# Kernel optimization log

Measured on AMD Instinct MI355X. Metric: run time of the kernel, lower is better.

The kernel has to match this reference:

```python
import jax, jax.numpy as jnp
import numpy as np

N_NODES = 100000
N_EDGES = 1600000
IN_F = 64
HID = 64
OUT_F = 64


def _param(key, shape, fan_in):
    return jax.random.normal(key, shape, dtype=jnp.float32) * (1.0 / np.sqrt(fan_in))


def setup_inputs() -> dict:
    key = jax.random.key(0)
    ks = jax.random.split(key, 12)
    features = jax.random.normal(ks[0], (N_NODES, IN_F), dtype=jnp.float32)
    src = jax.random.randint(ks[1], (N_EDGES,), 0, N_NODES, dtype=jnp.int32)
    dst = jax.random.randint(ks[2], (N_EDGES,), 0, N_NODES, dtype=jnp.int32)
    dims = [(IN_F, HID), (HID, HID), (HID, OUT_F)]
    inp = {"features": features, "src": src, "dst": dst}
    for i, (din, dout) in enumerate(dims):
        inp[f"W_self{i}"] = _param(ks[3 + 3 * i], (din, dout), din)
        inp[f"W_neigh{i}"] = _param(ks[4 + 3 * i], (din, dout), din)
        inp[f"b{i}"] = jnp.zeros((dout,), dtype=jnp.float32)
    return inp


def _sage_layer(h, src, dst, W_self, W_neigh, b, deg_inv, n_nodes, act):
    # mean aggregation over in-neighbors: gather src feats, segment-sum into dst
    msum = jax.ops.segment_sum(h[src], dst, num_segments=n_nodes)  # [N, d]
    h_neigh = msum * deg_inv  # mean (zero-degree nodes -> 0, matching DGL)
    out = h @ W_self + h_neigh @ W_neigh + b
    return jax.nn.relu(out) if act else out


def reference(features, src, dst, W_self0, W_neigh0, b0, W_self1, W_neigh1, b1, W_self2, W_neigh2, b2):
    n = features.shape[0]
    deg = jax.ops.segment_sum(jnp.ones((src.shape[0],), jnp.float32), dst, num_segments=n)
    deg_inv = (1.0 / jnp.maximum(deg, 1.0))[:, None]  # [N, 1]
    h = _sage_layer(features, src, dst, W_self0, W_neigh0, b0, deg_inv, n, act=True)
    h = _sage_layer(h, src, dst, W_self1, W_neigh1, b1, deg_inv, n, act=True)
    h = _sage_layer(h, src, dst, W_self2, W_neigh2, b2, deg_inv, n, act=False)
    return h
```

## Files before the change

### kernel.cpp

```cpp
#include <hip/hip_runtime.h>

#define NF 64
#define BUCKET 128
#define MAXB 8192
#define EPB 4096

typedef __attribute__((ext_vector_type(8))) short bf16x8;
typedef __attribute__((ext_vector_type(4))) float f32x4;

__device__ __forceinline__ float bf2f(unsigned short x) {
    union { unsigned int u; float f; } v; v.u = ((unsigned int)x) << 16; return v.f;
}
__device__ __forceinline__ unsigned short f2bf(float x) {
    union { float f; unsigned int u; } v; v.f = x;
    unsigned int r = (v.u + 0x7FFFu + ((v.u >> 16) & 1u)) >> 16;
    return (unsigned short)r;
}


__global__ __launch_bounds__(256) void bhist_kernel(const int* __restrict__ dst,
                                                    int* __restrict__ bins,
                                                    int n_edges, int nb) {
    __shared__ int h[MAXB];
    for (int i = threadIdx.x; i < nb; i += 256) h[i] = 0;
    __syncthreads();
    int base = blockIdx.x * EPB;
    int lim = min(base + EPB, n_edges);
    for (int i = base + threadIdx.x; i < lim; i += 256)
        atomicAdd(&h[dst[i] >> 7], 1);
    __syncthreads();
    for (int i = threadIdx.x; i < nb; i += 256) {
        int v = h[i];
        if (v) atomicAdd(&bins[i], v);
    }
}

__global__ __launch_bounds__(1024) void bscan_kernel(const int* __restrict__ bins,
                                                     int* __restrict__ bptr,
                                                     int* __restrict__ gcur, int nb) {
    __shared__ int sd[1024];
    int carry = 0;
    if (threadIdx.x == 0) bptr[0] = 0;
    for (int base = 0; base < nb; base += 1024) {
        int i = base + threadIdx.x;
        int v = (i < nb) ? bins[i] : 0;
        sd[threadIdx.x] = v;
        __syncthreads();
        for (int off = 1; off < 1024; off <<= 1) {
            int t = (threadIdx.x >= off) ? sd[threadIdx.x - off] : 0;
            __syncthreads();
            sd[threadIdx.x] += t;
            __syncthreads();
        }
        if (i < nb) {
            int ex = carry + sd[threadIdx.x] - v;
            bptr[i + 1] = carry + sd[threadIdx.x];
            gcur[i] = ex;
        }
        int last = sd[1023];
        __syncthreads();
        carry += last;
    }
}

__global__ __launch_bounds__(256) void bscatter_kernel(const int* __restrict__ src,
                                                       const int* __restrict__ dst,
                                                       int* __restrict__ gcur,
                                                       unsigned* __restrict__ bedges,
                                                       int n_edges, int nb) {
    __shared__ int h[MAXB];
    for (int i = threadIdx.x; i < nb; i += 256) h[i] = 0;
    __syncthreads();
    int base = blockIdx.x * EPB;
    int myDst[16], mySrc[16];
#pragma unroll
    for (int k = 0; k < 16; ++k) {
        int i = base + k * 256 + threadIdx.x;
        if (i < n_edges) {
            myDst[k] = dst[i];
            mySrc[k] = src[i];
            atomicAdd(&h[myDst[k] >> 7], 1);
        } else {
            myDst[k] = -1;
        }
    }
    __syncthreads();
    for (int i = threadIdx.x; i < nb; i += 256) {
        int v = h[i];
        h[i] = v ? atomicAdd(&gcur[i], v) : 0;
    }
    __syncthreads();
#pragma unroll
    for (int k = 0; k < 16; ++k) {
        if (myDst[k] >= 0) {
            int bin = myDst[k] >> 7;
            int pos = atomicAdd(&h[bin], 1);
            bedges[pos] = ((unsigned)mySrc[k] << 7) | (unsigned)(myDst[k] & 127);
        }
    }
}

__global__ __launch_bounds__(256) void bfinal_kernel(
    const unsigned* __restrict__ bedges, const int* __restrict__ bptr,
    int* __restrict__ row_ptr, float* __restrict__ deginv,
    int* __restrict__ col, int n_nodes, int n_edges, int nb) {
    __shared__ int cnt[BUCKET];
    __shared__ int sa[BUCKET], sb2[BUCKET];
    int tid = threadIdx.x;
    int b = blockIdx.x;
    int beg = bptr[b], end = bptr[b + 1];
    if (tid < BUCKET) cnt[tid] = 0;
    __syncthreads();
    for (int i = beg + tid; i < end; i += 256)
        atomicAdd(&cnt[bedges[i] & (BUCKET - 1)], 1);
    __syncthreads();
    if (tid < BUCKET) sa[tid] = cnt[tid];
    __syncthreads();
    int* pin = sa; int* pout = sb2;
    for (int off = 1; off < BUCKET; off <<= 1) {
        if (tid < BUCKET) pout[tid] = pin[tid] + ((tid >= off) ? pin[tid - off] : 0);
        __syncthreads();
        int* t = pin; pin = pout; pout = t;
    }
    int nodeBase = b * BUCKET;
    if (tid < BUCKET && nodeBase + tid < n_nodes) {
        row_ptr[nodeBase + tid] = beg + (tid ? pin[tid - 1] : 0);
        deginv[nodeBase + tid] = 1.0f / fmaxf((float)cnt[tid], 1.0f);
    }
    if (b == nb - 1 && tid == 0) row_ptr[n_nodes] = n_edges;
    __syncthreads();
    if (tid < BUCKET) cnt[tid] = 0;
    __syncthreads();
    for (int i = beg + tid; i < end; i += 256) {
        unsigned e = bedges[i];
        int d = e & (BUCKET - 1);
        int pos = beg + (d ? pin[d - 1] : 0) + atomicAdd(&cnt[d], 1);
        col[pos] = (int)(e >> 7);
    }
}


__global__ void convert_kernel(const float* __restrict__ in, unsigned short* __restrict__ X, int n_nodes) {
    int t = blockIdx.x * blockDim.x + threadIdx.x;
    int total = n_nodes * 16;
    if (t >= total) return;
    int n = t >> 4, g = t & 15;
    float4 v = *reinterpret_cast<const float4*>(in + (size_t)n * 64 + g * 4);
    ushort4 o;
    o.x = f2bf(v.x); o.y = f2bf(v.y); o.z = f2bf(v.z); o.w = f2bf(v.w);
    *reinterpret_cast<ushort4*>(X + (size_t)n * 128 + g * 4) = o;
}

__global__ void wtrans_kernel(const float* __restrict__ Ws, const float* __restrict__ Wn,
                              unsigned short* __restrict__ WT) {
    int t = blockIdx.x * blockDim.x + threadIdx.x;
    if (t >= 64 * 128) return;
    int j = t >> 7, k = t & 127;
    float v = (k < 64) ? Ws[k * 64 + j] : Wn[(k - 64) * 64 + j];
    WT[(size_t)j * 128 + k] = f2bf(v);
}

__global__ __launch_bounds__(256) void aggregate_bf16_kernel(
    unsigned short* __restrict__ X, const int* __restrict__ row_ptr, const int* __restrict__ col,
    const float* __restrict__ deginv, int n_nodes) {
    int lane = threadIdx.x & 63;
    int wid = threadIdx.x >> 6;
    int n = blockIdx.x * 4 + wid;
    if (n >= n_nodes) return;
    int beg = row_ptr[n], end = row_ptr[n + 1];
    float acc = 0.f;
    int i = beg;
    for (; i + 3 < end; i += 4) {
        int s0 = col[i], s1 = col[i + 1], s2 = col[i + 2], s3 = col[i + 3];
        float v0 = bf2f(X[(size_t)s0 * 128 + lane]);
        float v1 = bf2f(X[(size_t)s1 * 128 + lane]);
        float v2 = bf2f(X[(size_t)s2 * 128 + lane]);
        float v3 = bf2f(X[(size_t)s3 * 128 + lane]);
        acc += (v0 + v1) + (v2 + v3);
    }
    for (; i < end; ++i) acc += bf2f(X[(size_t)col[i] * 128 + lane]);
    X[(size_t)n * 128 + 64 + lane] = f2bf(acc * deginv[n]);
}

__global__ __launch_bounds__(256) void linear_mfma_kernel(
    const unsigned short* __restrict__ X, const unsigned short* __restrict__ WT,
    const float* __restrict__ bias, unsigned short* __restrict__ outBf,
    float* __restrict__ outF32, int n_nodes, int do_relu) {
    int lane = threadIdx.x & 63;
    int wid = threadIdx.x >> 6;
    int l15 = lane & 15;
    int lg = lane >> 4;

    bf16x8 wf[4][4];
#pragma unroll
    for (int ft = 0; ft < 4; ++ft)
#pragma unroll
        for (int ks = 0; ks < 4; ++ks)
            wf[ft][ks] = *reinterpret_cast<const bf16x8*>(
                WT + (size_t)(ft * 16 + l15) * 128 + ks * 32 + lg * 8);

    float4 bv[4];
#pragma unroll
    for (int ft = 0; ft < 4; ++ft)
        bv[ft] = *reinterpret_cast<const float4*>(bias + ft * 16 + lg * 4);

    int tiles = (n_nodes + 15) >> 4;
    for (int tile = blockIdx.x * 4 + wid; tile < tiles; tile += gridDim.x * 4) {
        int nodeBase = tile * 16;
        int nrow = nodeBase + l15;
        int rrow = nrow < n_nodes ? nrow : n_nodes - 1;

        bf16x8 xf[4];
#pragma unroll
        for (int ks = 0; ks < 4; ++ks)
            xf[ks] = *reinterpret_cast<const bf16x8*>(X + (size_t)rrow * 128 + ks * 32 + lg * 8);

        f32x4 acc[4];
#pragma unroll
        for (int ft = 0; ft < 4; ++ft) acc[ft] = (f32x4){0.f, 0.f, 0.f, 0.f};
#pragma unroll
        for (int ks = 0; ks < 4; ++ks) {
#pragma unroll
            for (int ft = 0; ft < 4; ++ft)
                acc[ft] = __builtin_amdgcn_mfma_f32_16x16x32_bf16(wf[ft][ks], xf[ks], acc[ft], 0, 0, 0);
        }

        if (nrow < n_nodes) {
#pragma unroll
            for (int ft = 0; ft < 4; ++ft) {
                float4 v;
                v.x = acc[ft][0] + bv[ft].x;
                v.y = acc[ft][1] + bv[ft].y;
                v.z = acc[ft][2] + bv[ft].z;
                v.w = acc[ft][3] + bv[ft].w;
                if (do_relu) {
                    v.x = fmaxf(v.x, 0.f); v.y = fmaxf(v.y, 0.f);
                    v.z = fmaxf(v.z, 0.f); v.w = fmaxf(v.w, 0.f);
                }
                int fbase = ft * 16 + lg * 4;
                if (outF32) {
                    *reinterpret_cast<float4*>(outF32 + (size_t)nrow * 64 + fbase) = v;
                } else {
                    ushort4 o;
                    o.x = f2bf(v.x); o.y = f2bf(v.y); o.z = f2bf(v.z); o.w = f2bf(v.w);
                    *reinterpret_cast<ushort4*>(outBf + (size_t)nrow * 128 + fbase) = o;
                }
            }
        }
    }
}


__global__ void deg_kernel(const int* __restrict__ dst, float* __restrict__ deg, int n_edges) {
    int e = blockIdx.x * blockDim.x + threadIdx.x;
    if (e < n_edges) unsafeAtomicAdd(&deg[dst[e]], 1.0f);
}

__global__ void inv_kernel(float* __restrict__ deg, int n) {
    int i = blockIdx.x * blockDim.x + threadIdx.x;
    if (i < n) deg[i] = 1.0f / fmaxf(deg[i], 1.0f);
}

__global__ __launch_bounds__(256) void scatter_kernel(
    const float* __restrict__ h, const int* __restrict__ src, const int* __restrict__ dst,
    float* __restrict__ agg, int n_edges) {
    int t = blockIdx.x * blockDim.x + threadIdx.x;
    int e = t >> 4;
    if (e >= n_edges) return;
    int q = (t & 15) * 4;
    int s = src[e];
    int d = dst[e];
    float4 v = *reinterpret_cast<const float4*>(h + (size_t)s * NF + q);
    float* o = agg + (size_t)d * NF + q;
    unsafeAtomicAdd(o + 0, v.x);
    unsafeAtomicAdd(o + 1, v.y);
    unsafeAtomicAdd(o + 2, v.z);
    unsafeAtomicAdd(o + 3, v.w);
}

__global__ __launch_bounds__(256) void linear_kernel(
    const float* __restrict__ h, const float* __restrict__ agg, const float* __restrict__ deginv,
    const float* __restrict__ Ws, const float* __restrict__ Wn, const float* __restrict__ bias,
    float* __restrict__ out, int n_nodes, int do_relu) {
    __shared__ float sWs[NF * NF];
    __shared__ float sWn[NF * NF];
    __shared__ float sb[NF];
    for (int i = threadIdx.x; i < NF * NF; i += 256) {
        sWs[i] = Ws[i];
        sWn[i] = Wn[i];
    }
    if (threadIdx.x < NF) sb[threadIdx.x] = bias[threadIdx.x];
    __syncthreads();
    int j = threadIdx.x & 63;
    int sub = threadIdx.x >> 6;
    for (int n = blockIdx.x * 4 + sub; n < n_nodes; n += gridDim.x * 4) {
        const float4* hr = reinterpret_cast<const float4*>(h + (size_t)n * NF);
        const float4* ar = reinterpret_cast<const float4*>(agg + (size_t)n * NF);
        float accS = 0.f, accN = 0.f;
#pragma unroll
        for (int k4 = 0; k4 < 16; ++k4) {
            float4 hv = hr[k4];
            float4 av = ar[k4];
            int kb = k4 * 4;
            accS += hv.x * sWs[(kb + 0) * NF + j];
            accN += av.x * sWn[(kb + 0) * NF + j];
            accS += hv.y * sWs[(kb + 1) * NF + j];
            accN += av.y * sWn[(kb + 1) * NF + j];
            accS += hv.z * sWs[(kb + 2) * NF + j];
            accN += av.z * sWn[(kb + 2) * NF + j];
            accS += hv.w * sWs[(kb + 3) * NF + j];
            accN += av.w * sWn[(kb + 3) * NF + j];
        }
        float val = accS + deginv[n] * accN + sb[j];
        if (do_relu) val = fmaxf(val, 0.f);
        out[(size_t)n * NF + j] = val;
    }
}


extern "C" void kernel_launch(void* const* d_in, const int* in_sizes, int n_in,
                              void* d_out, int out_size, void* d_ws, size_t ws_size,
                              hipStream_t stream) {
    const float* features = (const float*)d_in[0];
    const int* src = (const int*)d_in[1];
    const int* dst = (const int*)d_in[2];
    const float* Ws0 = (const float*)d_in[3];
    const float* Wn0 = (const float*)d_in[4];
    const float* b0  = (const float*)d_in[5];
    const float* Ws1 = (const float*)d_in[6];
    const float* Wn1 = (const float*)d_in[7];
    const float* b1  = (const float*)d_in[8];
    const float* Ws2 = (const float*)d_in[9];
    const float* Wn2 = (const float*)d_in[10];
    const float* b2  = (const float*)d_in[11];

    const int n_nodes = in_sizes[0] / NF;
    const int n_edges = in_sizes[1];
    float* out = (float*)d_out;

    const int nb = (n_nodes + BUCKET - 1) / BUCKET;
    const size_t alignNB = (((size_t)nb + 1) * 4 + 255) / 256 * 256;
    const size_t alignN = (((size_t)n_nodes + 64) * 4 + 255) / 256 * 256;
    const size_t alignE = ((size_t)n_edges * 4 + 255) / 256 * 256;
    const size_t xBytes = ((size_t)n_nodes * 128 * 2 + 255) / 256 * 256;
    const size_t wtBytes = 64 * 128 * 2;

    dim3 blk(256);
    const int nEB = (n_edges + EPB - 1) / EPB;
    const int waveBlocks = (n_nodes + 3) / 4;
    const int tiles = (n_nodes + 15) / 16;
    const int linBlocks = ((tiles + 3) / 4 < 640) ? (tiles + 3) / 4 : 640;

    const size_t need = 3 * alignNB + 2 * alignN + alignE + 2 * xBytes + 3 * wtBytes;
    const bool outFits = (size_t)out_size * sizeof(float) >= (size_t)n_edges * sizeof(unsigned);

    if (ws_size >= need && nb <= MAXB && n_nodes < (1 << 25) && outFits) {
        char* ws = (char*)d_ws;
        int* bins     = (int*)ws;
        int* bptr     = (int*)(ws + alignNB);
        int* gcur     = (int*)(ws + 2 * alignNB);
        int* row_ptr  = (int*)(ws + 3 * alignNB);
        float* deginv = (float*)(ws + 3 * alignNB + alignN);
        int* col      = (int*)(ws + 3 * alignNB + 2 * alignN);
        unsigned short* X0  = (unsigned short*)(ws + 3 * alignNB + 2 * alignN + alignE);
        unsigned short* X1  = (unsigned short*)((char*)X0 + xBytes);
        unsigned short* WT0 = (unsigned short*)((char*)X1 + xBytes);
        unsigned short* WT1 = WT0 + 64 * 128;
        unsigned short* WT2 = WT1 + 64 * 128;
        unsigned* bedges = (unsigned*)d_out;

        hipMemsetAsync(bins, 0, (size_t)nb * sizeof(int), stream);
        bhist_kernel<<<nEB, blk, 0, stream>>>(dst, bins, n_edges, nb);
        bscan_kernel<<<1, 1024, 0, stream>>>(bins, bptr, gcur, nb);
        bscatter_kernel<<<nEB, blk, 0, stream>>>(src, dst, gcur, bedges, n_edges, nb);
        bfinal_kernel<<<nb, blk, 0, stream>>>(bedges, bptr, row_ptr, deginv, col, n_nodes, n_edges, nb);

        convert_kernel<<<(n_nodes * 16 + 255) / 256, blk, 0, stream>>>(features, X0, n_nodes);
        wtrans_kernel<<<32, blk, 0, stream>>>(Ws0, Wn0, WT0);
        wtrans_kernel<<<32, blk, 0, stream>>>(Ws1, Wn1, WT1);
        wtrans_kernel<<<32, blk, 0, stream>>>(Ws2, Wn2, WT2);

        aggregate_bf16_kernel<<<waveBlocks, blk, 0, stream>>>(X0, row_ptr, col, deginv, n_nodes);
        linear_mfma_kernel<<<linBlocks, blk, 0, stream>>>(X0, WT0, b0, X1, nullptr, n_nodes, 1);
        aggregate_bf16_kernel<<<waveBlocks, blk, 0, stream>>>(X1, row_ptr, col, deginv, n_nodes);
        linear_mfma_kernel<<<linBlocks, blk, 0, stream>>>(X1, WT1, b1, X0, nullptr, n_nodes, 1);
        aggregate_bf16_kernel<<<waveBlocks, blk, 0, stream>>>(X0, row_ptr, col, deginv, n_nodes);
        linear_mfma_kernel<<<linBlocks, blk, 0, stream>>>(X0, WT2, b2, nullptr, out, n_nodes, 0);
    } else {
        char* ws = (char*)d_ws;
        size_t degBytes = (((size_t)n_nodes * 4) + 255) / 256 * 256;
        float* deg = (float*)ws;
        float* agg = (float*)(ws + degBytes);
        float* h1  = agg + (size_t)n_nodes * NF;
        int scatBlocks = (n_edges * 16 + 255) / 256;
        int eBlocks = (n_edges + 255) / 256;
        size_t rowBytes = (size_t)n_nodes * NF * sizeof(float);

        hipMemsetAsync(deg, 0, (size_t)n_nodes * sizeof(float), stream);
        deg_kernel<<<eBlocks, blk, 0, stream>>>(dst, deg, n_edges);
        inv_kernel<<<(n_nodes + 255) / 256, blk, 0, stream>>>(deg, n_nodes);

        hipMemsetAsync(agg, 0, rowBytes, stream);
        scatter_kernel<<<scatBlocks, blk, 0, stream>>>(features, src, dst, agg, n_edges);
        linear_kernel<<<waveBlocks, blk, 0, stream>>>(features, agg, deg, Ws0, Wn0, b0, out, n_nodes, 1);

        hipMemsetAsync(agg, 0, rowBytes, stream);
        scatter_kernel<<<scatBlocks, blk, 0, stream>>>(out, src, dst, agg, n_edges);
        linear_kernel<<<waveBlocks, blk, 0, stream>>>(out, agg, deg, Ws1, Wn1, b1, h1, n_nodes, 1);

        hipMemsetAsync(agg, 0, rowBytes, stream);
        scatter_kernel<<<scatBlocks, blk, 0, stream>>>(h1, src, dst, agg, n_edges);
        linear_kernel<<<waveBlocks, blk, 0, stream>>>(h1, agg, deg, Ws2, Wn2, b2, out, n_nodes, 0);
    }
}
```

Before: 312.6 us.

## Vectorize neighbor gather in aggregation with 4 edges per wave step

The per-node aggregation used to have each lane load one bf16 element per edge. It now has 16 lanes read 8-byte ushort4 chunks of a row, so each wave instruction fetches four edges at once with 16 edges per iteration, then combines partial sums with cross-lane shuffles. This cuts the number of load instructions and raises memory-level parallelism for the gather. It adds shuffle reductions and predication for tail edges. The linear kernel grid cap of 640 blocks is also removed, so it launches one block per four tiles.

```diff
diff --git a/kernel.cpp b/kernel.cpp
--- a/kernel.cpp
+++ b/kernel.cpp
@@ -165,21 +165,44 @@
     const float* __restrict__ deginv, int n_nodes) {
     int lane = threadIdx.x & 63;
     int wid = threadIdx.x >> 6;
+    int q = lane >> 4;
+    int j = lane & 15;
     int n = blockIdx.x * 4 + wid;
     if (n >= n_nodes) return;
     int beg = row_ptr[n], end = row_ptr[n + 1];
-    float acc = 0.f;
-    int i = beg;
-    for (; i + 3 < end; i += 4) {
-        int s0 = col[i], s1 = col[i + 1], s2 = col[i + 2], s3 = col[i + 3];
-        float v0 = bf2f(X[(size_t)s0 * 128 + lane]);
-        float v1 = bf2f(X[(size_t)s1 * 128 + lane]);
-        float v2 = bf2f(X[(size_t)s2 * 128 + lane]);
-        float v3 = bf2f(X[(size_t)s3 * 128 + lane]);
-        acc += (v0 + v1) + (v2 + v3);
-    }
-    for (; i < end; ++i) acc += bf2f(X[(size_t)col[i] * 128 + lane]);
-    X[(size_t)n * 128 + 64 + lane] = f2bf(acc * deginv[n]);
+    float a0 = 0.f, a1 = 0.f, a2 = 0.f, a3 = 0.f;
+    for (int i = beg; i < end; i += 16) {
+        ushort4 v[4];
+        int ok[4];
+#pragma unroll
+        for (int u = 0; u < 4; ++u) {
+            int eidx = i + u * 4 + q;
+            ok[u] = eidx < end;
+            int ei = ok[u] ? eidx : end - 1;
+            int s = col[ei];
+            v[u] = *reinterpret_cast<const ushort4*>(X + (size_t)s * 128 + j * 4);
+        }
+#pragma unroll
+        for (int u = 0; u < 4; ++u) {
+            if (ok[u]) {
+                a0 += bf2f(v[u].x);
+                a1 += bf2f(v[u].y);
+                a2 += bf2f(v[u].z);
+                a3 += bf2f(v[u].w);
+            }
+        }
+    }
+    a0 += __shfl_xor(a0, 16); a1 += __shfl_xor(a1, 16);
+    a2 += __shfl_xor(a2, 16); a3 += __shfl_xor(a3, 16);
+    a0 += __shfl_xor(a0, 32); a1 += __shfl_xor(a1, 32);
+    a2 += __shfl_xor(a2, 32); a3 += __shfl_xor(a3, 32);
+    if (q == 0) {
+        float dinv = deginv[n];
+        ushort4 o;
+        o.x = f2bf(a0 * dinv); o.y = f2bf(a1 * dinv);
+        o.z = f2bf(a2 * dinv); o.w = f2bf(a3 * dinv);
+        *reinterpret_cast<ushort4*>(X + (size_t)n * 128 + 64 + j * 4) = o;
+    }
 }
 
 __global__ __launch_bounds__(256) void linear_mfma_kernel(
@@ -349,7 +372,7 @@
     const int nEB = (n_edges + EPB - 1) / EPB;
     const int waveBlocks = (n_nodes + 3) / 4;
     const int tiles = (n_nodes + 15) / 16;
-    const int linBlocks = ((tiles + 3) / 4 < 640) ? (tiles + 3) / 4 : 640;
+    const int linBlocks = (tiles + 3) / 4;
 
     const size_t need = 3 * alignNB + 2 * alignN + alignE + 2 * xBytes + 3 * wtBytes;
     const bool outFits = (size_t)out_size * sizeof(float) >= (size_t)n_edges * sizeof(unsigned);
```

After: 273.3 us. 1.14x faster.

## Vectorize bf16 neighbor gather with 16-byte loads and drop deginv buffer

Applied to the files above, without the earlier changes.

The aggregation kernel now has each wave process 8 neighbors at once, with 8 lanes each loading a 16-byte chunk of a neighbor row. Partial sums are reduced with cross-lane shuffles, replacing the one-bf16-per-lane scalar gathers. The degree inverse is computed inline from row_ptr instead of read from a separate array, and the three weight-transpose launches are merged into one. The linear kernel grid is no longer capped at 640 blocks. In exchange the gather adds shuffle-reduction overhead, and predicated lanes are wasted on nodes with few neighbors.

```diff
diff --git a/kernel.cpp b/kernel.cpp
--- a/kernel.cpp
+++ b/kernel.cpp
@@ -7,6 +7,7 @@
 
 typedef __attribute__((ext_vector_type(8))) short bf16x8;
 typedef __attribute__((ext_vector_type(4))) float f32x4;
+typedef __attribute__((ext_vector_type(4))) unsigned int u32x4;
 
 __device__ __forceinline__ float bf2f(unsigned short x) {
     union { unsigned int u; float f; } v; v.u = ((unsigned int)x) << 16; return v.f;
@@ -102,8 +103,8 @@
 
 __global__ __launch_bounds__(256) void bfinal_kernel(
     const unsigned* __restrict__ bedges, const int* __restrict__ bptr,
-    int* __restrict__ row_ptr, float* __restrict__ deginv,
-    int* __restrict__ col, int n_nodes, int n_edges, int nb) {
+    int* __restrict__ row_ptr, int* __restrict__ col,
+    int n_nodes, int n_edges, int nb) {
     __shared__ int cnt[BUCKET];
     __shared__ int sa[BUCKET], sb2[BUCKET];
     int tid = threadIdx.x;
@@ -123,10 +124,8 @@
         int* t = pin; pin = pout; pout = t;
     }
     int nodeBase = b * BUCKET;
-    if (tid < BUCKET && nodeBase + tid < n_nodes) {
+    if (tid < BUCKET && nodeBase + tid < n_nodes)
         row_ptr[nodeBase + tid] = beg + (tid ? pin[tid - 1] : 0);
-        deginv[nodeBase + tid] = 1.0f / fmaxf((float)cnt[tid], 1.0f);
-    }
     if (b == nb - 1 && tid == 0) row_ptr[n_nodes] = n_edges;
     __syncthreads();
     if (tid < BUCKET) cnt[tid] = 0;
@@ -151,35 +150,70 @@
     *reinterpret_cast<ushort4*>(X + (size_t)n * 128 + g * 4) = o;
 }
 
-__global__ void wtrans_kernel(const float* __restrict__ Ws, const float* __restrict__ Wn,
+__global__ void wtrans_kernel(const float* __restrict__ Ws0, const float* __restrict__ Wn0,
+                              const float* __restrict__ Ws1, const float* __restrict__ Wn1,
+                              const float* __restrict__ Ws2, const float* __restrict__ Wn2,
                               unsigned short* __restrict__ WT) {
     int t = blockIdx.x * blockDim.x + threadIdx.x;
-    if (t >= 64 * 128) return;
-    int j = t >> 7, k = t & 127;
+    if (t >= 3 * 64 * 128) return;
+    int layer = t >> 13;
+    int r = t & 8191;
+    int j = r >> 7, k = r & 127;
+    const float* Ws = layer == 0 ? Ws0 : (layer == 1 ? Ws1 : Ws2);
+    const float* Wn = layer == 0 ? Wn0 : (layer == 1 ? Wn1 : Wn2);
     float v = (k < 64) ? Ws[k * 64 + j] : Wn[(k - 64) * 64 + j];
-    WT[(size_t)j * 128 + k] = f2bf(v);
+    WT[t] = f2bf(v);
 }
 
 __global__ __launch_bounds__(256) void aggregate_bf16_kernel(
     unsigned short* __restrict__ X, const int* __restrict__ row_ptr, const int* __restrict__ col,
-    const float* __restrict__ deginv, int n_nodes) {
+    int n_nodes) {
     int lane = threadIdx.x & 63;
     int wid = threadIdx.x >> 6;
+    int q = lane >> 3;
+    int j = lane & 7;
     int n = blockIdx.x * 4 + wid;
     if (n >= n_nodes) return;
     int beg = row_ptr[n], end = row_ptr[n + 1];
-    float acc = 0.f;
-    int i = beg;
-    for (; i + 3 < end; i += 4) {
-        int s0 = col[i], s1 = col[i + 1], s2 = col[i + 2], s3 = col[i + 3];
-        float v0 = bf2f(X[(size_t)s0 * 128 + lane]);
-        float v1 = bf2f(X[(size_t)s1 * 128 + lane]);
-        float v2 = bf2f(X[(size_t)s2 * 128 + lane]);
-        float v3 = bf2f(X[(size_t)s3 * 128 + lane]);
-        acc += (v0 + v1) + (v2 + v3);
-    }
-    for (; i < end; ++i) acc += bf2f(X[(size_t)col[i] * 128 + lane]);
-    X[(size_t)n * 128 + 64 + lane] = f2bf(acc * deginv[n]);
+    float a[8] = {0.f, 0.f, 0.f, 0.f, 0.f, 0.f, 0.f, 0.f};
+    for (int i = beg; i < end; i += 16) {
+        int e0 = i + q, e1 = i + 8 + q;
+        bool ok0 = e0 < end, ok1 = e1 < end;
+        int s0 = col[ok0 ? e0 : end - 1];
+        int s1 = col[ok1 ? e1 : end - 1];
+        u32x4 v0 = *reinterpret_cast<const u32x4*>(X + (size_t)s0 * 128 + j * 8);
+        u32x4 v1 = *reinterpret_cast<const u32x4*>(X + (size_t)s1 * 128 + j * 8);
+        if (ok0) {
+#pragma unroll
+            for (int k = 0; k < 4; ++k) {
+                union { unsigned u; float f; } lo, hi;
+                lo.u = v0[k] << 16; hi.u = v0[k] & 0xffff0000u;
+                a[2 * k] += lo.f; a[2 * k + 1] += hi.f;
+            }
+        }
+        if (ok1) {
+#pragma unroll
+            for (int k = 0; k < 4; ++k) {
+                union { unsigned u; float f; } lo, hi;
+                lo.u = v1[k] << 16; hi.u = v1[k] & 0xffff0000u;
+                a[2 * k] += lo.f; a[2 * k + 1] += hi.f;
+            }
+        }
+    }
+#pragma unroll
+    for (int k = 0; k < 8; ++k) {
+        a[k] += __shfl_xor(a[k], 8);
+        a[k] += __shfl_xor(a[k], 16);
+        a[k] += __shfl_xor(a[k], 32);
+    }
+    if (q == 0) {
+        float dinv = 1.0f / fmaxf((float)(end - beg), 1.0f);
+        u32x4 o;
+#pragma unroll
+        for (int k = 0; k < 4; ++k)
+            o[k] = ((unsigned)f2bf(a[2 * k + 1] * dinv) << 16) | f2bf(a[2 * k] * dinv);
+        *reinterpret_cast<u32x4*>(X + (size_t)n * 128 + 64 + j * 8) = o;
+    }
 }
 
 __global__ __launch_bounds__(256) void linear_mfma_kernel(
@@ -343,15 +377,15 @@
     const size_t alignN = (((size_t)n_nodes + 64) * 4 + 255) / 256 * 256;
     const size_t alignE = ((size_t)n_edges * 4 + 255) / 256 * 256;
     const size_t xBytes = ((size_t)n_nodes * 128 * 2 + 255) / 256 * 256;
-    const size_t wtBytes = 64 * 128 * 2;
+    const size_t wtBytes = 3 * 64 * 128 * 2;
 
     dim3 blk(256);
     const int nEB = (n_edges + EPB - 1) / EPB;
     const int waveBlocks = (n_nodes + 3) / 4;
     const int tiles = (n_nodes + 15) / 16;
-    const int linBlocks = ((tiles + 3) / 4 < 640) ? (tiles + 3) / 4 : 640;
-
-    const size_t need = 3 * alignNB + 2 * alignN + alignE + 2 * xBytes + 3 * wtBytes;
+    const int linBlocks = (tiles + 3) / 4;
+
+    const size_t need = 3 * alignNB + alignN + alignE + 2 * xBytes + wtBytes;
     const bool outFits = (size_t)out_size * sizeof(float) >= (size_t)n_edges * sizeof(unsigned);
 
     if (ws_size >= need && nb <= MAXB && n_nodes < (1 << 25) && outFits) {
@@ -360,31 +394,29 @@
         int* bptr     = (int*)(ws + alignNB);
         int* gcur     = (int*)(ws + 2 * alignNB);
         int* row_ptr  = (int*)(ws + 3 * alignNB);
-        float* deginv = (float*)(ws + 3 * alignNB + alignN);
-        int* col      = (int*)(ws + 3 * alignNB + 2 * alignN);
-        unsigned short* X0  = (unsigned short*)(ws + 3 * alignNB + 2 * alignN + alignE);
+        int* col      = (int*)(ws + 3 * alignNB + alignN);
+        unsigned short* X0  = (unsigned short*)(ws + 3 * alignNB + alignN + alignE);
         unsigned short* X1  = (unsigned short*)((char*)X0 + xBytes);
-        unsigned short* WT0 = (unsigned short*)((char*)X1 + xBytes);
-        unsigned short* WT1 = WT0 + 64 * 128;
-        unsigned short* WT2 = WT1 + 64 * 128;
+        unsigned short* WT  = (unsigned short*)((char*)X1 + xBytes);
+        unsigned short* WT0 = WT;
+        unsigned short* WT1 = WT + 64 * 128;
+        unsigned short* WT2 = WT + 2 * 64 * 128;
         unsigned* bedges = (unsigned*)d_out;
 
         hipMemsetAsync(bins, 0, (size_t)nb * sizeof(int), stream);
         bhist_kernel<<<nEB, blk, 0, stream>>>(dst, bins, n_edges, nb);
         bscan_kernel<<<1, 1024, 0, stream>>>(bins, bptr, gcur, nb);
         bscatter_kernel<<<nEB, blk, 0, stream>>>(src, dst, gcur, bedges, n_edges, nb);
-        bfinal_kernel<<<nb, blk, 0, stream>>>(bedges, bptr, row_ptr, deginv, col, n_nodes, n_edges, nb);
+        bfinal_kernel<<<nb, blk, 0, stream>>>(bedges, bptr, row_ptr, col, n_nodes, n_edges, nb);
 
         convert_kernel<<<(n_nodes * 16 + 255) / 256, blk, 0, stream>>>(features, X0, n_nodes);
-        wtrans_kernel<<<32, blk, 0, stream>>>(Ws0, Wn0, WT0);
-        wtrans_kernel<<<32, blk, 0, stream>>>(Ws1, Wn1, WT1);
-        wtrans_kernel<<<32, blk, 0, stream>>>(Ws2, Wn2, WT2);
-
-        aggregate_bf16_kernel<<<waveBlocks, blk, 0, stream>>>(X0, row_ptr, col, deginv, n_nodes);
+        wtrans_kernel<<<96, blk, 0, stream>>>(Ws0, Wn0, Ws1, Wn1, Ws2, Wn2, WT);
+
+        aggregate_bf16_kernel<<<waveBlocks, blk, 0, stream>>>(X0, row_ptr, col, n_nodes);
         linear_mfma_kernel<<<linBlocks, blk, 0, stream>>>(X0, WT0, b0, X1, nullptr, n_nodes, 1);
-        aggregate_bf16_kernel<<<waveBlocks, blk, 0, stream>>>(X1, row_ptr, col, deginv, n_nodes);
+        aggregate_bf16_kernel<<<waveBlocks, blk, 0, stream>>>(X1, row_ptr, col, n_nodes);
         linear_mfma_kernel<<<linBlocks, blk, 0, stream>>>(X1, WT1, b1, X0, nullptr, n_nodes, 1);
-        aggregate_bf16_kernel<<<waveBlocks, blk, 0, stream>>>(X0, row_ptr, col, deginv, n_nodes);
+        aggregate_bf16_kernel<<<waveBlocks, blk, 0, stream>>>(X0, row_ptr, col, n_nodes);
         linear_mfma_kernel<<<linBlocks, blk, 0, stream>>>(X0, WT2, b2, nullptr, out, n_nodes, 0);
     } else {
         char* ws = (char*)d_ws;
```

Measured after the change: 258.7 us. -17.3%, faster.
